# Optimization experiments

Measured on AMD Instinct MI355X. Metric: run time of the kernel, lower is better.

Reference implementation:

```python
import jax, jax.numpy as jnp
import numpy as np

N_NODES = 100000
MAX_DEG = 128
NODE_DIM = 256
BATCH = 4096
NUM_SAMPLES = 32


def setup_inputs() -> dict:
    key = jax.random.key(0)
    k1, k2, k3, k4 = jax.random.split(key, 4)
    adj_info = jax.random.randint(k1, (N_NODES, MAX_DEG), 0, N_NODES, dtype=jnp.int32)
    features = jax.random.normal(k2, (N_NODES, NODE_DIM), dtype=jnp.float32)
    ids = jax.random.randint(k3, (BATCH,), 0, N_NODES, dtype=jnp.int32)
    W = jax.random.normal(k4, (NODE_DIM, NODE_DIM), dtype=jnp.float32) * 0.05
    b = jnp.zeros((NODE_DIM,), jnp.float32)
    return {"adj_info": adj_info, "features": features, "ids": ids,
            "W": W, "b": b, "num_samples": NUM_SAMPLES}


def reference(adj_info, features, ids, W, b, num_samples):
    # adj_info: [n_nodes, neig_num] int32; features: [n_nodes, D]
    V = ids.shape[0]
    neig_num = adj_info.shape[1]
    group_dim = neig_num // num_samples
    n_keep = group_dim * num_samples

    adj_lists = adj_info[ids][:, :n_keep]          # [V, N] gather
    v_f = features[ids]                            # [V, D]
    n_f = features[adj_lists]                      # [V, N, D] gather

    # linear sampler branch: dense(v_f) then matmul against neighbor features
    l = v_f @ W + b                                # [V, D]
    scores = jax.nn.relu(jnp.einsum('vd,vnd->vn', l, n_f))  # [V, N]

    # grouped argmin: neighbor index = s*group_dim + argmin within group
    scores = scores.reshape(V, num_samples, group_dim)
    idx_y = jnp.argmin(scores, axis=-1).astype(jnp.int32)   # [V, S]
    idx_y = idx_y + (jnp.arange(num_samples, dtype=jnp.int32) * group_dim)[None, :]

    sel = jnp.take_along_axis(adj_lists, idx_y, axis=1)     # [V, S]

    # count non-dummy neighbors (dummy id = n_nodes - 1)
    is_dummy = sel == (adj_info.shape[0] - 1)
    adj_lists_numnz = jnp.sum(jnp.where(is_dummy, 0.0, 1.0), axis=1)  # [V]
    att_lists = jnp.ones((V, num_samples), jnp.float32)
    dummy_ = adj_lists_numnz
    return sel, att_lists, adj_lists_numnz, dummy_
```

## Files before the change

### kernel.cpp

```cpp
#include <hip/hip_runtime.h>
#include <hip/hip_bf16.h>


constexpr int D        = 256;
constexpr int V        = 4096;
constexpr int MAXDEG   = 128;
constexpr int S        = 32;
constexpr int DUMMY_ID = 99999;

constexpr int OFF_SEL  = 0;
constexpr int OFF_ATT  = V * S;
constexpr int OFF_NNZ  = 2 * V * S;
constexpr int OFF_DMY  = 2 * V * S + V;

__device__ __forceinline__ float bf16_round_f32(float f) {
    unsigned int u = __float_as_uint(f);
    u += 0x7FFFu + ((u >> 16) & 1u);
    u &= 0xFFFF0000u;
    return __uint_as_float(u);
}

__global__ __launch_bounds__(256) void fused_k(
    const int* __restrict__ adj, const float* __restrict__ features,
    const int* __restrict__ ids, const float* __restrict__ W,
    const float* __restrict__ bias, float* __restrict__ out)
{
    const int v    = blockIdx.x;
    const int tid  = threadIdx.x;
    const int lane = tid & 63;
    const int wave = tid >> 6;

    __shared__ float  vf[D];
    __shared__ double lsh[D];
    __shared__ int cnt;
    if (tid == 0) cnt = 0;

    const int node = ids[v];
    vf[tid] = features[(size_t)node * D + tid];
    __syncthreads();

    double acc = (double)bias[tid];
    #pragma unroll 4
    for (int d = 0; d < D; ++d)
        acc = fma((double)vf[d], (double)W[d * D + tid], acc);
    lsh[tid] = acc;
    __syncthreads();

    const double2 lv01 = *reinterpret_cast<const double2*>(&lsh[lane * 4]);
    const double2 lv23 = *reinterpret_cast<const double2*>(&lsh[lane * 4 + 2]);
    const int* arow = adj + (size_t)node * MAXDEG + wave * 32;

    double best  = 0.0;
    int    bestn = 0;
    int    localcnt = 0;

    for (int n = 0; n < 32; ++n) {
        const int nb = arow[n];
        const float4 f = *reinterpret_cast<const float4*>(features + (size_t)nb * D + lane * 4);
        double p = fma((double)lv01.x, (double)f.x,
                   fma((double)lv01.y, (double)f.y,
                   fma((double)lv23.x, (double)f.z,
                       (double)lv23.y * (double)f.w)));
        #pragma unroll
        for (int off = 32; off; off >>= 1) p += __shfl_xor(p, off);
        const double s = fmax(p, 0.0);

        const int g = n & 3;
        if (g == 0)          { best = s; bestn = n; }
        else if (s < best)   { best = s; bestn = n; }

        if (g == 3 && lane == 0) {
            const int sample = wave * 8 + (n >> 2);
            const int selid  = arow[bestn];
            out[OFF_SEL + v * S + sample] = bf16_round_f32((float)selid);
            out[OFF_ATT + v * S + sample] = 1.0f;
            if (selid != DUMMY_ID) ++localcnt;
        }
    }

    if (lane == 0 && localcnt) atomicAdd(&cnt, localcnt);
    __syncthreads();
    if (tid == 0) {
        const float c = (float)cnt;
        out[OFF_NNZ + v] = c;
        out[OFF_DMY + v] = c;
    }
}

extern "C" void kernel_launch(void* const* d_in, const int* in_sizes, int n_in,
                              void* d_out, int out_size, void* d_ws, size_t ws_size,
                              hipStream_t stream)
{
    const int*   adj      = (const int*)d_in[0];
    const float* features = (const float*)d_in[1];
    const int*   ids      = (const int*)d_in[2];
    const float* W        = (const float*)d_in[3];
    const float* bias     = (const float*)d_in[4];
    (void)d_ws; (void)ws_size;

    float* out = (float*)d_out;

    fused_k<<<V, 256, 0, stream>>>(adj, features, ids, W, bias, out);
}
```

Measured before the change: 295.7 us.

## Process four batch rows per block and assign one neighbor per lane

Each block now handles four batch rows. Every W element loaded feeds the four dense-layer dot products, which cuts W traffic fourfold. The neighbor-scoring phase gives each wave one row and each lane a whole neighbor (two per lane), so the per-neighbor 64-lane shuffle reduction becomes a thread-local dot product plus a 4-lane argmin shuffle, and the counting uses ballot instead of shared atomics. The risk is that each lane now reads a full feature row, so accesses within a wave are strided rather than coalesced, and the grid has fewer blocks.

After: 289.3 us. 2.1% less time.

```diff
diff --git a/kernel.cpp b/kernel.cpp
--- a/kernel.cpp
+++ b/kernel.cpp
@@ -25,63 +25,128 @@
     const int* __restrict__ ids, const float* __restrict__ W,
     const float* __restrict__ bias, float* __restrict__ out)
 {
-    const int v    = blockIdx.x;
     const int tid  = threadIdx.x;
     const int lane = tid & 63;
     const int wave = tid >> 6;
+    const int v0   = blockIdx.x * 4;
 
-    __shared__ float  vf[D];
-    __shared__ double lsh[D];
-    __shared__ int cnt;
-    if (tid == 0) cnt = 0;
+    __shared__ float  vf[4][D];
+    __shared__ double lsh[4][D];
 
-    const int node = ids[v];
-    vf[tid] = features[(size_t)node * D + tid];
+    const int node0 = ids[v0 + 0];
+    const int node1 = ids[v0 + 1];
+    const int node2 = ids[v0 + 2];
+    const int node3 = ids[v0 + 3];
+
+    vf[0][tid] = features[(size_t)node0 * D + tid];
+    vf[1][tid] = features[(size_t)node1 * D + tid];
+    vf[2][tid] = features[(size_t)node2 * D + tid];
+    vf[3][tid] = features[(size_t)node3 * D + tid];
+
+    if (tid < 4 * S) out[OFF_ATT + v0 * S + tid] = 1.0f;
     __syncthreads();
 
-    double acc = (double)bias[tid];
-    #pragma unroll 4
-    for (int d = 0; d < D; ++d)
-        acc = fma((double)vf[d], (double)W[d * D + tid], acc);
-    lsh[tid] = acc;
+    double a[4][4];
+    {
+        const double b0 = (double)bias[tid];
+        #pragma unroll
+        for (int vi = 0; vi < 4; ++vi) {
+            a[vi][0] = (vi == vi) ? 0.0 : 0.0;
+            a[vi][1] = 0.0; a[vi][2] = 0.0; a[vi][3] = 0.0;
+        }
+        a[0][0] = b0; a[1][0] = b0; a[2][0] = b0; a[3][0] = b0;
+        #pragma unroll 2
+        for (int d = 0; d < D; d += 4) {
+            const double w0 = (double)W[(d    ) * D + tid];
+            const double w1 = (double)W[(d + 1) * D + tid];
+            const double w2 = (double)W[(d + 2) * D + tid];
+            const double w3 = (double)W[(d + 3) * D + tid];
+            #pragma unroll
+            for (int vi = 0; vi < 4; ++vi) {
+                a[vi][0] = fma((double)vf[vi][d    ], w0, a[vi][0]);
+                a[vi][1] = fma((double)vf[vi][d + 1], w1, a[vi][1]);
+                a[vi][2] = fma((double)vf[vi][d + 2], w2, a[vi][2]);
+                a[vi][3] = fma((double)vf[vi][d + 3], w3, a[vi][3]);
+            }
+        }
+        #pragma unroll
+        for (int vi = 0; vi < 4; ++vi)
+            lsh[vi][tid] = (a[vi][0] + a[vi][1]) + (a[vi][2] + a[vi][3]);
+    }
     __syncthreads();
 
-    const double2 lv01 = *reinterpret_cast<const double2*>(&lsh[lane * 4]);
-    const double2 lv23 = *reinterpret_cast<const double2*>(&lsh[lane * 4 + 2]);
-    const int* arow = adj + (size_t)node * MAXDEG + wave * 32;
+    const int v    = v0 + wave;
+    const int node = (wave == 0) ? node0 : (wave == 1) ? node1 : (wave == 2) ? node2 : node3;
+    const int* arow = adj + (size_t)node * MAXDEG;
 
-    double best  = 0.0;
-    int    bestn = 0;
-    int    localcnt = 0;
+    const int nb0 = arow[lane];
+    const int nb1 = arow[64 + lane];
+    const float* r0 = features + (size_t)nb0 * D;
+    const float* r1 = features + (size_t)nb1 * D;
+    const double* lrow = lsh[wave];
 
-    for (int n = 0; n < 32; ++n) {
-        const int nb = arow[n];
-        const float4 f = *reinterpret_cast<const float4*>(features + (size_t)nb * D + lane * 4);
-        double p = fma((double)lv01.x, (double)f.x,
-                   fma((double)lv01.y, (double)f.y,
-                   fma((double)lv23.x, (double)f.z,
-                       (double)lv23.y * (double)f.w)));
-        #pragma unroll
-        for (int off = 32; off; off >>= 1) p += __shfl_xor(p, off);
-        const double s = fmax(p, 0.0);
+    double p0a = 0.0, p0b = 0.0, p0c = 0.0, p0d = 0.0;
+    double p1a = 0.0, p1b = 0.0, p1c = 0.0, p1d = 0.0;
 
-        const int g = n & 3;
-        if (g == 0)          { best = s; bestn = n; }
-        else if (s < best)   { best = s; bestn = n; }
+    #pragma unroll 2
+    for (int d = 0; d < D; d += 8) {
+        const double2 la = *reinterpret_cast<const double2*>(&lrow[d    ]);
+        const double2 lb = *reinterpret_cast<const double2*>(&lrow[d + 2]);
+        const double2 lc = *reinterpret_cast<const double2*>(&lrow[d + 4]);
+        const double2 ld = *reinterpret_cast<const double2*>(&lrow[d + 6]);
+        const float4 x0 = *reinterpret_cast<const float4*>(r0 + d);
+        const float4 x1 = *reinterpret_cast<const float4*>(r0 + d + 4);
+        const float4 y0 = *reinterpret_cast<const float4*>(r1 + d);
+        const float4 y1 = *reinterpret_cast<const float4*>(r1 + d + 4);
 
-        if (g == 3 && lane == 0) {
-            const int sample = wave * 8 + (n >> 2);
-            const int selid  = arow[bestn];
-            out[OFF_SEL + v * S + sample] = bf16_round_f32((float)selid);
-            out[OFF_ATT + v * S + sample] = 1.0f;
-            if (selid != DUMMY_ID) ++localcnt;
-        }
+        p0a = fma(la.x, (double)x0.x, p0a);
+        p0b = fma(la.y, (double)x0.y, p0b);
+        p0c = fma(lb.x, (double)x0.z, p0c);
+        p0d = fma(lb.y, (double)x0.w, p0d);
+        p0a = fma(lc.x, (double)x1.x, p0a);
+        p0b = fma(lc.y, (double)x1.y, p0b);
+        p0c = fma(ld.x, (double)x1.z, p0c);
+        p0d = fma(ld.y, (double)x1.w, p0d);
+
+        p1a = fma(la.x, (double)y0.x, p1a);
+        p1b = fma(la.y, (double)y0.y, p1b);
+        p1c = fma(lb.x, (double)y0.z, p1c);
+        p1d = fma(lb.y, (double)y0.w, p1d);
+        p1a = fma(lc.x, (double)y1.x, p1a);
+        p1b = fma(lc.y, (double)y1.y, p1b);
+        p1c = fma(ld.x, (double)y1.z, p1c);
+        p1d = fma(ld.y, (double)y1.w, p1d);
     }
 
-    if (lane == 0 && localcnt) atomicAdd(&cnt, localcnt);
-    __syncthreads();
-    if (tid == 0) {
-        const float c = (float)cnt;
+    double s0 = fmax((p0a + p0b) + (p0c + p0d), 0.0);
+    double s1 = fmax((p1a + p1b) + (p1c + p1d), 0.0);
+
+    int pos0 = lane & 3, id0 = nb0;
+    int pos1 = lane & 3, id1 = nb1;
+    #pragma unroll
+    for (int off = 1; off < 4; off <<= 1) {
+        const double so0 = __shfl_xor(s0, off);
+        const int    po0 = __shfl_xor(pos0, off);
+        const int    io0 = __shfl_xor(id0, off);
+        if (so0 < s0 || (so0 == s0 && po0 < pos0)) { s0 = so0; pos0 = po0; id0 = io0; }
+
+        const double so1 = __shfl_xor(s1, off);
+        const int    po1 = __shfl_xor(pos1, off);
+        const int    io1 = __shfl_xor(id1, off);
+        if (so1 < s1 || (so1 == s1 && po1 < pos1)) { s1 = so1; pos1 = po1; id1 = io1; }
+    }
+
+    const bool winner = (lane & 3) == 0;
+    if (winner) {
+        const int g = lane >> 2;
+        out[OFF_SEL + v * S + g     ] = bf16_round_f32((float)id0);
+        out[OFF_SEL + v * S + 16 + g] = bf16_round_f32((float)id1);
+    }
+
+    const unsigned long long b0 = __ballot(winner && (id0 != DUMMY_ID));
+    const unsigned long long b1 = __ballot(winner && (id1 != DUMMY_ID));
+    if (lane == 0) {
+        const float c = (float)(__popcll(b0) + __popcll(b1));
         out[OFF_NNZ + v] = c;
         out[OFF_DMY + v] = c;
     }
@@ -100,5 +165,5 @@
 
     float* out = (float*)d_out;
 
-    fused_k<<<V, 256, 0, stream>>>(adj, features, ids, W, bias, out);
+    fused_k<<<V / 4, 256, 0, stream>>>(adj, features, ids, W, bias, out);
 }
```

## Process two nodes per block and give each lane a whole neighbor dot product

Applied to the files above, without the earlier changes.

Each block now handles two batch nodes, so every W value loaded in the dense layer feeds both nodes and W traffic is halved. The neighbor scoring changes from one wave cooperatively reducing each neighbor with shuffles to one lane computing the full 256-wide dot product for its own neighbor. A 4-lane shuffle argmin then picks the group winner, with ties going to the lower position. Per-lane row reads are strided rather than coalesced across the wave, and fewer, heavier blocks are launched.

Measured after the change: 270.9 us. 8.4% less time.

```diff
diff --git a/kernel.cpp b/kernel.cpp
--- a/kernel.cpp
+++ b/kernel.cpp
@@ -20,70 +20,96 @@
     return __uint_as_float(u);
 }
 
-__global__ __launch_bounds__(256) void fused_k(
+__global__ __launch_bounds__(256, 8) void fused_k(
     const int* __restrict__ adj, const float* __restrict__ features,
     const int* __restrict__ ids, const float* __restrict__ W,
     const float* __restrict__ bias, float* __restrict__ out)
 {
-    const int v    = blockIdx.x;
     const int tid  = threadIdx.x;
     const int lane = tid & 63;
     const int wave = tid >> 6;
+    const int v0   = blockIdx.x * 2;
 
-    __shared__ float  vf[D];
-    __shared__ double lsh[D];
-    __shared__ int cnt;
-    if (tid == 0) cnt = 0;
+    __shared__ float  vf[2][D];
+    __shared__ double lsh[2][D];
+    __shared__ int    cnt2[2];
 
-    const int node = ids[v];
-    vf[tid] = features[(size_t)node * D + tid];
+    if (tid < 2) cnt2[tid] = 0;
+
+    const int node0 = ids[v0 + 0];
+    const int node1 = ids[v0 + 1];
+    vf[0][tid] = features[(size_t)node0 * D + tid];
+    vf[1][tid] = features[(size_t)node1 * D + tid];
+
+    if (tid < 2 * S) out[OFF_ATT + v0 * S + tid] = 1.0f;
     __syncthreads();
 
-    double acc = (double)bias[tid];
-    #pragma unroll 4
-    for (int d = 0; d < D; ++d)
-        acc = fma((double)vf[d], (double)W[d * D + tid], acc);
-    lsh[tid] = acc;
+    {
+        const double b0 = (double)bias[tid];
+        double a00 = b0, a01 = 0.0, a02 = 0.0, a03 = 0.0;
+        double a10 = b0, a11 = 0.0, a12 = 0.0, a13 = 0.0;
+        #pragma unroll 2
+        for (int d = 0; d < D; d += 4) {
+            const double w0 = (double)W[(d    ) * D + tid];
+            const double w1 = (double)W[(d + 1) * D + tid];
+            const double w2 = (double)W[(d + 2) * D + tid];
+            const double w3 = (double)W[(d + 3) * D + tid];
+            a00 = fma((double)vf[0][d    ], w0, a00);
+            a01 = fma((double)vf[0][d + 1], w1, a01);
+            a02 = fma((double)vf[0][d + 2], w2, a02);
+            a03 = fma((double)vf[0][d + 3], w3, a03);
+            a10 = fma((double)vf[1][d    ], w0, a10);
+            a11 = fma((double)vf[1][d + 1], w1, a11);
+            a12 = fma((double)vf[1][d + 2], w2, a12);
+            a13 = fma((double)vf[1][d + 3], w3, a13);
+        }
+        lsh[0][tid] = (a00 + a01) + (a02 + a03);
+        lsh[1][tid] = (a10 + a11) + (a12 + a13);
+    }
     __syncthreads();
 
-    const double2 lv01 = *reinterpret_cast<const double2*>(&lsh[lane * 4]);
-    const double2 lv23 = *reinterpret_cast<const double2*>(&lsh[lane * 4 + 2]);
-    const int* arow = adj + (size_t)node * MAXDEG + wave * 32;
+    const int vh = wave >> 1;
+    const int h  = wave & 1;
+    const int v  = v0 + vh;
+    const int node = vh ? node1 : node0;
 
-    double best  = 0.0;
-    int    bestn = 0;
-    int    localcnt = 0;
+    const int nb = adj[(size_t)node * MAXDEG + h * 64 + lane];
+    const float*  r    = features + (size_t)nb * D;
+    const double* lrow = lsh[vh];
 
-    for (int n = 0; n < 32; ++n) {
-        const int nb = arow[n];
-        const float4 f = *reinterpret_cast<const float4*>(features + (size_t)nb * D + lane * 4);
-        double p = fma((double)lv01.x, (double)f.x,
-                   fma((double)lv01.y, (double)f.y,
-                   fma((double)lv23.x, (double)f.z,
-                       (double)lv23.y * (double)f.w)));
-        #pragma unroll
-        for (int off = 32; off; off >>= 1) p += __shfl_xor(p, off);
-        const double s = fmax(p, 0.0);
+    double pa = 0.0, pb = 0.0, pc = 0.0, pd = 0.0;
+    #pragma unroll 4
+    for (int d = 0; d < D; d += 4) {
+        const float4  x  = *reinterpret_cast<const float4*>(r + d);
+        const double2 e0 = *reinterpret_cast<const double2*>(&lrow[d]);
+        const double2 e1 = *reinterpret_cast<const double2*>(&lrow[d + 2]);
+        pa = fma(e0.x, (double)x.x, pa);
+        pb = fma(e0.y, (double)x.y, pb);
+        pc = fma(e1.x, (double)x.z, pc);
+        pd = fma(e1.y, (double)x.w, pd);
+    }
+    double s = fmax((pa + pb) + (pc + pd), 0.0);
 
-        const int g = n & 3;
-        if (g == 0)          { best = s; bestn = n; }
-        else if (s < best)   { best = s; bestn = n; }
-
-        if (g == 3 && lane == 0) {
-            const int sample = wave * 8 + (n >> 2);
-            const int selid  = arow[bestn];
-            out[OFF_SEL + v * S + sample] = bf16_round_f32((float)selid);
-            out[OFF_ATT + v * S + sample] = 1.0f;
-            if (selid != DUMMY_ID) ++localcnt;
-        }
+    int pos = lane & 3, id = nb;
+    #pragma unroll
+    for (int off = 1; off < 4; off <<= 1) {
+        const double so = __shfl_xor(s, off);
+        const int    po = __shfl_xor(pos, off);
+        const int    io = __shfl_xor(id, off);
+        if (so < s || (so == s && po < pos)) { s = so; pos = po; id = io; }
     }
 
-    if (lane == 0 && localcnt) atomicAdd(&cnt, localcnt);
+    const bool winner = (lane & 3) == 0;
+    if (winner)
+        out[OFF_SEL + v * S + h * 16 + (lane >> 2)] = bf16_round_f32((float)id);
+
+    const unsigned long long bal = __ballot(winner && (id != DUMMY_ID));
+    if (lane == 0) atomicAdd(&cnt2[vh], __popcll(bal));
     __syncthreads();
-    if (tid == 0) {
-        const float c = (float)cnt;
-        out[OFF_NNZ + v] = c;
-        out[OFF_DMY + v] = c;
+    if (tid < 2) {
+        const float c = (float)cnt2[tid];
+        out[OFF_NNZ + v0 + tid] = c;
+        out[OFF_DMY + v0 + tid] = c;
     }
 }
 
@@ -100,5 +126,5 @@
 
     float* out = (float*)d_out;
 
-    fused_k<<<V, 256, 0, stream>>>(adj, features, ids, W, bias, out);
+    fused_k<<<V / 2, 256, 0, stream>>>(adj, features, ids, W, bias, out);
 }
```
